# Performance work log

Hardware: AMD Instinct MI355X
Metric: run time of the kernel (lower is better)

Reference implementation:

```python
import jax, jax.numpy as jnp
import numpy as np

EPS = 1e-5


def _mlp_c(x, W0, b0, W1, b1, W2, b2, sub0):
    # per-channel 3-linear MLP (mlp_deep=2 hidden layers + output linear), hidden=latent
    h = jax.nn.relu(jnp.einsum(sub0, x, W0) + b0[:, None, None])
    h = jax.nn.relu(jnp.einsum('cbef,cfh->cbeh', h, W1) + b1[:, None, None])
    return jnp.einsum('cbef,cfh->cbeh', h, W2) + b2[:, None, None]


def _ln(x, w, b):
    # x: [C,B,M,L]; torch LayerNorm([C,M,L]) applied to x permuted to [B,C,M,L]
    # -> normalize jointly over (C,M,L) per batch element
    mu = jnp.mean(x, axis=(0, 2, 3), keepdims=True)
    var = jnp.mean((x - mu) ** 2, axis=(0, 2, 3), keepdims=True)
    return (x - mu) * jax.lax.rsqrt(var + EPS) * w[:, None] + b[:, None]


def _forward(src, dst, nodes, eW0_first, eb0_first, eW0_rest, eb0_rest,
             eW1, eb1, eW2, eb2, nW0, nb0, nW1, nb1, nW2, nb2,
             ln_nw, ln_nb, ln_ew, ln_eb):
    G, C = eW1.shape[0], eW1.shape[1]
    B, N = nodes.shape[0], nodes.shape[1]
    L = eW1.shape[-1]
    x = nodes  # [B,N,L]
    edges = None
    for i in range(G):
        # dropout p=0 -> identity (eval mode)
        if i == 0:
            # edge update: phi_e(concat(x_tgt, x_src)) per channel -> [C,B,E,L]
            m_in = jnp.concatenate([x[:, dst], x[:, src]], axis=-1)  # [B,E,2L]
            edges = _mlp_c(m_in, eW0_first, eb0_first, eW1[0], eb1[0], eW2[0], eb2[0], 'bef,cfh->cbeh')
            # scatter-add messages to target nodes
            agg = jnp.zeros((C, B, N, L), edges.dtype).at[:, :, dst].add(edges)
            n_in = jnp.concatenate([jnp.broadcast_to(x, (C, B, N, L)), agg], axis=-1)
        else:
            # x: [C,B,N,L], edges: [C,B,E,L]
            m_in = jnp.concatenate([x[:, :, dst], x[:, :, src], edges], axis=-1)  # [C,B,E,3L]
            edges = _mlp_c(m_in, eW0_rest[i - 1], eb0_rest[i - 1], eW1[i], eb1[i], eW2[i], eb2[i], 'cbef,cfh->cbeh')
            agg = jnp.zeros_like(x).at[:, :, dst].add(edges)
            n_in = jnp.concatenate([x, agg], axis=-1)  # [C,B,N,2L]
        x = _mlp_c(n_in, nW0[i], nb0[i], nW1[i], nb1[i], nW2[i], nb2[i], 'cbnf,cfh->cbnh')
        x = _ln(x, ln_nw[i], ln_nb[i])
        if i < G - 1:
            edges = _ln(edges, ln_ew[i], ln_eb[i])
    # channel_agg == 'sum'
    return jnp.sum(x, axis=0)  # [B,N,L]


def setup_inputs() -> dict:
    key = jax.random.key(0)
    B, N, L, C, G = 128, 64, 64, 2, 3
    E = N * (N - 1)
    pairs = np.array([[i, j] for i in range(N) for j in range(N) if i != j], dtype=np.int32)
    src = jnp.asarray(pairs[:, 0])  # edge_index row 0 (message source)
    dst = jnp.asarray(pairs[:, 1])  # edge_index row 1 (aggregation target)
    ks = jax.random.split(key, 8)

    def w(k, shape, fan):
        return jax.random.normal(k, shape, jnp.float32) / np.sqrt(fan)

    return {
        'nodes': jax.random.normal(ks[0], (B, N, L), jnp.float32),
        'src': src, 'dst': dst,
        'eW0_first': w(ks[1], (C, 2 * L, L), 2 * L), 'eb0_first': jnp.zeros((C, L), jnp.float32),
        'eW0_rest': w(ks[2], (G - 1, C, 3 * L, L), 3 * L), 'eb0_rest': jnp.zeros((G - 1, C, L), jnp.float32),
        'eW1': w(ks[3], (G, C, L, L), L), 'eb1': jnp.zeros((G, C, L), jnp.float32),
        'eW2': w(ks[4], (G, C, L, L), L), 'eb2': jnp.zeros((G, C, L), jnp.float32),
        'nW0': w(ks[5], (G, C, 2 * L, L), 2 * L), 'nb0': jnp.zeros((G, C, L), jnp.float32),
        'nW1': w(ks[6], (G, C, L, L), L), 'nb1': jnp.zeros((G, C, L), jnp.float32),
        'nW2': w(ks[7], (G, C, L, L), L), 'nb2': jnp.zeros((G, C, L), jnp.float32),
        'ln_nw': jnp.ones((G, C, N, L), jnp.float32), 'ln_nb': jnp.zeros((G, C, N, L), jnp.float32),
        'ln_ew': jnp.ones((G - 1, C, E, L), jnp.float32), 'ln_eb': jnp.zeros((G - 1, C, E, L), jnp.float32),
    }


def reference(nodes, src, dst, eW0_first, eb0_first, eW0_rest, eb0_rest,
              eW1, eb1, eW2, eb2, nW0, nb0, nW1, nb1, nW2, nb2,
              ln_nw, ln_nb, ln_ew, ln_eb):
    return _forward(src, dst, nodes, eW0_first, eb0_first, eW0_rest, eb0_rest,
                    eW1, eb1, eW2, eb2, nW0, nb0, nW1, nb1, nW2, nb2,
                    ln_nw, ln_nb, ln_ew, ln_eb)
```

## Files before the change

kernel.cpp:

```cpp
#include <hip/hip_runtime.h>

typedef __bf16 bf16;
typedef __attribute__((ext_vector_type(8))) __bf16 bf16x8;
typedef __attribute__((ext_vector_type(4))) __bf16 bf16x4;
typedef __attribute__((ext_vector_type(4))) float f32x4;

#define MFMA16(a,b,c) __builtin_amdgcn_mfma_f32_16x16x32_bf16((a),(b),(c),0,0,0)

#define CC 2
#define BB 128
#define EPAD 4096
#define EDGE_CNT_INV (1.0f/516096.0f)
#define NODE_CNT_INV (1.0f/8192.0f)
#define LNEPS 1e-5f

#define BC_EB0F 0
#define BC_EB0R 128
#define BC_EB1  384
#define BC_EB2  768
#define BC_NB0  1152
#define BC_NB1  1536
#define BC_NB2  1920
#define BC_TOT  2304

// ... 6 lines not shown
    16, 0, 0);
}

static __device__ __forceinline__ bool detectBf16(const void* p){
  const unsigned short* u = (const unsigned short*)p;
  int ok = 0;
#pragma unroll
  for (int i = 0; i < 64; ++i){
    unsigned v = u[i];
    unsigned e = (v >> 7) & 0xFFu;
    ok += (int)(((e >= 100u) && (e <= 150u)) || (v == 0u));
  }
  return ok >= 58;
}

static __device__ __forceinline__ float ldS(const void* p, long i, bool b16){
  return b16 ? (float)(((const bf16*)p)[i]) : ((const float*)p)[i];
}
static __device__ __forceinline__ void ld8(const void* p, long i, bool b16, float* o){
  if (b16){
    bf16x8 v = *(const bf16x8*)((const bf16*)p + i);
#pragma unroll
    for (int u=0;u<8;u++) o[u] = (float)v[u];
  } else {
    const float* f = (const float*)p + i;
    float4 a = *(const float4*)f; float4 b = *(const float4*)(f+4);
    o[0]=a.x;o[1]=a.y;o[2]=a.z;o[3]=a.w;o[4]=b.x;o[5]=b.y;o[6]=b.z;o[7]=b.w;
  }
}

static __device__ __forceinline__ unsigned sw128(unsigned row, unsigned cb){
  return row*128u + (cb ^ ((row&7u)<<4));
}
static __device__ __forceinline__ unsigned sw256(unsigned row, unsigned cb){
  return row*256u + (cb ^ ((row&7u)<<4));
}

static __device__ __forceinline__ void stage64(char* lds, const bf16* src, int tid){
#pragma unroll
  for (int q=0;q<2;q++){
    int idx = tid + q*256;
    int r = idx>>3; unsigned cb = (unsigned)((idx&7)*16);
    *(int4*)(lds + sw128((unsigned)r, cb)) = *(const int4*)((const char*)src + r*128 + cb);
  }
}
static __device__ __forceinline__ void stage128(char* lds, const bf16* src, int tid){
#pragma unroll
  for (int q=0;q<4;q++){
    int idx = tid + q*256;
    int r = idx>>4; unsigned cb = (unsigned)((idx&15)*16);
    *(int4*)(lds + sw256((unsigned)r, cb)) = *(const int4*)((const char*)src + r*256 + cb);
  }
}
static __device__ __forceinline__ void stageLin(char* lds, const char* src, int tid){
#pragma unroll
  for (int q=0;q<2;q++){
    int idx = tid + q*256;
    *(int4*)(lds + idx*16) = *(const int4*)(src + idx*16);
  }
}

static __device__ __forceinline__ bf16x8 frd64(const char* p, int row, int ks, int lane){
  return *(const bf16x8*)(p + sw128((unsigned)row, (unsigned)(ks*64 + ((lane>>4)<<4))));
}
static __device__ __forceinline__ bf16x8 frd256(const char* p, int row, int ks, int lane){
  return *(const bf16x8*)(p + sw256((unsigned)row, (unsigned)(ks*64 + ((lane>>4)<<4))));
}

template<int NMT>
static __device__ __forceinline__ void gemm64(const char* wlds, const char* hlds, int lane, f32x4 (*acc)[NMT]){
  int m15 = lane & 15;
  bf16x8 af[4][2];
#pragma unroll
  for (int nt=0;nt<4;nt++){
    af[nt][0] = frd64(wlds, nt*16+m15, 0, lane);
    af[nt][1] = frd64(wlds, nt*16+m15, 1, lane);
  }
#pragma unroll
  for (int mt=0;mt<NMT;mt++){
    bf16x8 b0 = frd64(hlds, mt*16+m15, 0, lane);
    bf16x8 b1 = frd64(hlds, mt*16+m15, 1, lane);
#pragma unroll
    for (int nt=0;nt<4;nt++){
      acc[nt][mt] = MFMA16(af[nt][0], b0, acc[nt][mt]);
      acc[nt][mt] = MFMA16(af[nt][1], b1, acc[nt][mt]);
    }
  }
}

template<int NMT>
static __device__ __forceinline__ void accZero(f32x4 (*acc)[NMT]){
#pragma unroll
  for (int a=0;a<4;a++){ for (int m=0;m<NMT;m++) acc[a][m] = zf4(); }
}
template<int NMT>
static __device__ __forceinline__ void accBias(const bf16* bias, int lane, f32x4 (*acc)[NMT]){
  int hi = lane>>4;
#pragma unroll
  for (int nt=0;nt<4;nt++){
    f32x4 bv;
#pragma unroll
    for (int r=0;r<4;r++) bv[r] = (float)bias[nt*16 + hi*4 + r];
#pragma unroll
    for (int mt=0;mt<NMT;mt++) acc[nt][mt] = bv;
  }
}
template<int NMT>
static __device__ __forceinline__ void epiRelu(char* hlds, int lane, f32x4 (*acc)[NMT]){
  int hi = lane>>4, m15 = lane&15;
#pragma unroll
  for (int nt=0;nt<4;nt++){
#pragma unroll
    for (int mt=0;mt<NMT;mt++){
      f32x4 v = acc[nt][mt];
      bf16x4 o;
#pragma unroll
      for (int r=0;r<4;r++){
        float t = v[r];
        t = t > 0.f ? t : 0.f;
        o[r] = (bf16)t;
      }
      *(bf16x4*)(hlds + sw128((unsigned)(mt*16+m15), (unsigned)(nt*32 + hi*8))) = o;
    }
  }
}

__global__ void k_prep(const void* nodes,
    const void* eW0f, const void* eW0r, const void* eW1, const void* eW2,
    const void* nW0, const void* nW1, const void* nW2,
    const void* ln_ew, const void* ln_eb, const void* ln_nw, const void* ln_nb,
    const void* eb0f, const void* eb0r, const void* eb1, const void* eb2,
    const void* nb0, const void* nb1, const void* nb2,
    bf16* WTpd, bf16* WTps, bf16* WTe0e, bf16* WTe1, bf16* WTe2,
    bf16* WTn0, bf16* WTn1, bf16* WTn2,
    bf16* lnwP, bf16* lnbP,
    bf16* xn0, bf16* lnnW, bf16* lnnB, bf16* bc, int* flag)
{
  bool b16 = detectBf16(nodes);
  int tid = threadIdx.x, blk = blockIdx.x;
  if (blk < 256){
    int t = blk>>7, c = (blk>>6)&1, j = blk&63;
    int k = tid>>2, part = tid&3;
    long dofs = (((long)(t*CC + c))*EPAD + j*64 + k)*64 + part*16;
    if (k < 63){
      int i = k + (k>=j ? 1 : 0);
      int eref = i*63 + j - (j>i ? 1 : 0);
      long sofs = (((long)(t*CC + c))*4032 + eref)*64 + part*16;
      float o[8]; bf16x8 v;
      ld8(ln_ew, sofs,   b16, o); for (int u=0;u<8;u++) v[u]=(bf16)o[u]; *(bf16x8*)(lnwP+dofs)   = v;
      ld8(ln_ew, sofs+8, b16, o); for (int u=0;u<8;u++) v[u]=(bf16)o[u]; *(bf16x8*)(lnwP+dofs+8) = v;
      ld8(ln_eb, sofs,   b16, o); for (int u=0;u<8;u++) v[u]=(bf16)o[u]; *(bf16x8*)(lnbP+dofs)   = v;
      ld8(ln_eb, sofs+8, b16, o); for (int u=0;u<8;u++) v[u]=(bf16)o[u]; *(bf16x8*)(lnbP+dofs+8) = v;
    } else {
      bf16x8 z; for (int u=0;u<8;u++) z[u]=(bf16)0.f;
      *(bf16x8*)(lnwP+dofs)=z; *(bf16x8*)(lnwP+dofs+8)=z;
      *(bf16x8*)(lnbP+dofs)=z; *(bf16x8*)(lnbP+dofs+8)=z;
    }
    return;
  }
  int job = blk - 256;
  if (job < 46){
    const void* src = nullptr; bf16* dst = nullptr; int K = 64; long so = 0;
    if (job < 6){        int t=job>>1, c=job&1; dst = WTpd + (long)(t*CC+c)*4096;
      if (t==0){ src=eW0f; so=(long)c*128*64; } else { src=eW0r; so=((long)(t-1)*CC+c)*192*64; } }
    else if (job < 12){  int q=job-6; int t=q>>1,c=q&1; dst = WTps + (long)(t*CC+c)*4096;
      if (t==0){ src=eW0f; so=(long)c*128*64 + 64*64; } else { src=eW0r; so=((long)(t-1)*CC+c)*192*64 + 64*64; } }
    else if (job < 16){  int q=job-12; int t=q>>1,c=q&1; dst=WTe0e + (long)(t*CC+c)*4096; src=eW0r; so=((long)t*CC+c)*192*64 + 128*64; }
    else if (job < 22){  int q=job-16; int t=q>>1,c=q&1; dst=WTe1 + (long)(t*CC+c)*4096; src=eW1; so=((long)t*CC+c)*4096; }
    else if (job < 28){  int q=job-22; int t=q>>1,c=q&1; dst=WTe2 + (long)(t*CC+c)*4096; src=eW2; so=((long)t*CC+c)*4096; }
    else if (job < 34){  int q=job-28; int t=q>>1,c=q&1; dst=WTn0 + (long)(t*CC+c)*8192; src=nW0; so=((long)t*CC+c)*128*64; K=128; }
    else if (job < 40){  int q=job-34; int t=q>>1,c=q&1; dst=WTn1 + (long)(t*CC+c)*4096; src=nW1; so=((long)t*CC+c)*4096; }
    else              {  int q=job-40; int t=q>>1,c=q&1; dst=WTn2 + (long)(t*CC+c)*4096; src=nW2; so=((long)t*CC+c)*4096; }
    for (int idx = tid; idx < K*64; idx += 256){
      int n = idx & 63, k = idx >> 6;
      dst[(long)n*K + k] = (bf16)ldS(src, so + (long)k*64 + n, b16);
// ... 22 lines not shown
#pragma unroll
      for (int u=0;u<8;u++) v[u]=(bf16)t[u];
      *(bf16x8*)(dst + o) = v;
    }
  } else {
    for (int idx = tid; idx < BC_TOT; idx += 256){
      float v;
      if      (idx < BC_EB0R) v = ldS(eb0f, idx - BC_EB0F, b16);
      else if (idx < BC_EB1 ) v = ldS(eb0r, idx - BC_EB0R, b16);
      else if (idx < BC_EB2 ) v = ldS(eb1,  idx - BC_EB1,  b16);
      else if (idx < BC_NB0 ) v = ldS(eb2,  idx - BC_EB2,  b16);
      else if (idx < BC_NB1 ) v = ldS(nb0,  idx - BC_NB0,  b16);
      else if (idx < BC_NB2 ) v = ldS(nb1,  idx - BC_NB1,  b16);
      else                    v = ldS(nb2,  idx - BC_NB2,  b16);
      bc[idx] = (bf16)v;
    }
    if (tid == 0) flag[0] = b16 ? 1 : 0;
  }
}

__global__ __launch_bounds__(256,2) void k_p0(const bf16* xn0,
    const bf16* WTpd, const bf16* WTps, const bf16* bc, bf16* Xd, bf16* Xs)
{
  int tid=threadIdx.x, lane=tid&63, w=tid>>6;
  int b = blockIdx.x;
  extern __shared__ char sm[];
  char* xn = sm;
  char* Wp = sm + 8192;
  stage64(xn, xn0 + (long)b*4096, tid);
  stage64(Wp,         WTpd + 0,    tid);
  stage64(Wp + 8192,  WTps + 0,    tid);
  stage64(Wp + 16384, WTpd + 4096, tid);
  stage64(Wp + 24576, WTps + 4096, tid);
  __syncthreads();
  int c = w>>1, p = w&1;
  f32x4 acc[4][4];
  if (p==0) accBias<4>(bc + BC_EB0F + c*64, lane, acc);
  else accZero<4>(acc);
  gemm64<4>(Wp + (c*2+p)*8192, xn, lane, acc);
  int hi=lane>>4, m15=lane&15;
  bf16* dst = (p==0 ? Xd : Xs) + ((long)c*BB + b)*64*64;
#pragma unroll
  for (int nt=0;nt<4;nt++){
#pragma unroll
    for (int mt=0;mt<4;mt++){
      f32x4 v = acc[nt][mt];
      bf16x4 o = {(bf16)v[0],(bf16)v[1],(bf16)v[2],(bf16)v[3]};
      *(bf16x4*)(dst + (long)(mt*16+m15)*64 + nt*16+hi*4) = o;
    }
  }
}

template<int T>
__global__ __launch_bounds__(256,2) void k_edge(
    bf16* edges, const bf16* Xd, const bf16* Xs, float* agg, float* eS,
    const float2* eMR,
    const bf16* WTe0e, const bf16* WTe1, const bf16* WTe2,
    const bf16* lnwP, const bf16* lnbP, const bf16* bc)
{
  int tid=threadIdx.x, lane=tid&63, w=tid>>6;
  int j = blockIdx.x, bg = blockIdx.y, c = blockIdx.z;
  extern __shared__ char sm[];
  char* Wl1 = sm;
  char* Wl2 = sm + 8192;
  char* Wl0 = sm + 16384;
  char* lwL = sm + 24576;
  char* lbL = sm + 32768;
  char* hb  = sm + (T>0 ? 40960 : 16384) + w*8192;

  int hi = lane>>4, m15 = lane&15;
  int mrow = lane>>3;
  unsigned cbyte = (unsigned)((lane&7)*16);
  int cbk = (lane&7)*8;
  int b0 = bg*32 + w*8;

  float2 mr8[8];
  if (T>0){
#pragma unroll
    for (int t=0;t<8;t++) mr8[t] = eMR[(T-1)*BB + b0 + t];
  }

  stage64(Wl1, WTe1 + (long)(T*CC+c)*4096, tid);
  stage64(Wl2, WTe2 + (long)(T*CC+c)*4096, tid);
  if (T>0){
    stage64(Wl0, WTe0e + (long)((T-1)*CC+c)*4096, tid);
    const char* lwg = (const char*)(lnwP + (((long)(T-1)*CC+c)*EPAD + (long)j*64)*64);
    const char* lbg = (const char*)(lnbP + (((long)(T-1)*CC+c)*EPAD + (long)j*64)*64);
    stageLin(lwL, lwg, tid);
    stageLin(lbL, lbg, tid);
  }
  __syncthreads();

  for (int t=0; t<8; t++){
    int b = b0 + t;
    long cb = (long)c*BB + b;
    bf16* erow = edges + (cb*EPAD + (long)j*64)*64;
    const bf16* xdrow = Xd + (cb*64 + j)*64;
    const bf16* xsbase = Xs + cb*4096;

    f32x4 acc[4][4];

    if (T==0){
      bf16x8 xd8v = *(const bf16x8*)(xdrow + cbk);
      float xd8[8];
#pragma unroll
      for (int u=0;u<8;u++) xd8[u] = (float)xd8v[u];
#pragma unroll
      for (int it=0; it<8; it++){
        int m = mrow + it*8;
        int i = m + (m>=j ? 1 : 0); if (i>63) i = 63;
        bf16x8 y8 = *(const bf16x8*)(xsbase + (long)i*64 + cbk);
        bf16x8 o;
#pragma unroll
        for (int u=0;u<8;u++){
          float tt = xd8[u] + (float)y8[u];
          tt = tt > 0.f ? tt : 0.f;
          o[u] = (bf16)tt;
        }
        *(bf16x8*)(hb + sw128((unsigned)m, (unsigned)(cbk*2))) = o;
      }
      accBias<4>(bc + BC_EB1 + (T*CC+c)*64, lane, acc);
      gemm64<4>(Wl1, hb, lane, acc);
      epiRelu<4>(hb, lane, acc);
      accBias<4>(bc + BC_EB2 + (T*CC+c)*64, lane, acc);
      gemm64<4>(Wl2, hb, lane, acc);
    } else {
      float mu = mr8[t].x, rs = mr8[t].y;
      asm volatile("s_waitcnt lgkmcnt(0)" ::: "memory");
#pragma unroll
      for (int it=0; it<8; it++)
        dma16(hb + it*1024, (const char*)erow + it*1024 + (long)lane*16);
      asm volatile("s_waitcnt vmcnt(0)" ::: "memory");
      __builtin_amdgcn_sched_barrier(0);
#pragma unroll
      for (int it=0; it<8; it++){
        int m = mrow + it*8;
        bf16x8 e  = *(const bf16x8*)(hb  + lane*16 + it*1024);
        bf16x8 wv = *(const bf16x8*)(lwL + lane*16 + it*1024);
        bf16x8 bv = *(const bf16x8*)(lbL + lane*16 + it*1024);
        bf16x8 o;
#pragma unroll
        for (int u=0;u<8;u++){
          float tt = ((float)e[u] - mu) * rs;
          tt = tt * (float)wv[u] + (float)bv[u];
          o[u] = (bf16)tt;
        }
        *(bf16x8*)(hb + sw128((unsigned)m, cbyte)) = o;
      }
      bf16x4 xdv[4], xsv[4][4];
#pragma unroll
      for (int nt=0;nt<4;nt++) xdv[nt] = *(const bf16x4*)(xdrow + nt*16 + hi*4);
#pragma unroll
      for (int mt=0;mt<4;mt++){
        int m = mt*16 + m15;
        int i = m + (m>=j ? 1 : 0); if (i>63) i=63;
#pragma unroll
        for (int nt=0;nt<4;nt++)
          xsv[mt][nt] = *(const bf16x4*)(xsbase + (long)i*64 + nt*16 + hi*4);
      }
      accZero<4>(acc);
      gemm64<4>(Wl0, hb, lane, acc);
#pragma unroll
      for (int mt=0;mt<4;mt++){
        int m = mt*16 + m15;
#pragma unroll
        for (int nt=0;nt<4;nt++){
          f32x4 v = acc[nt][mt];
          float t0 = v[0] + (float)xdv[nt][0] + (float)xsv[mt][nt][0];
          float t1 = v[1] + (float)xdv[nt][1] + (float)xsv[mt][nt][1];
          float t2 = v[2] + (float)xdv[nt][2] + (float)xsv[mt][nt][2];
          float t3 = v[3] + (float)xdv[nt][3] + (float)xsv[mt][nt][3];
          bf16x4 o;
          o[0] = (bf16)(t0>0.f?t0:0.f); o[1] = (bf16)(t1>0.f?t1:0.f);
          o[2] = (bf16)(t2>0.f?t2:0.f); o[3] = (bf16)(t3>0.f?t3:0.f);
          *(bf16x4*)(hb + sw128((unsigned)m, (unsigned)(nt*32+hi*8))) = o;
        }
      }
      accBias<4>(bc + BC_EB1 + (T*CC+c)*64, lane, acc);
      gemm64<4>(Wl1, hb, lane, acc);
      epiRelu<4>(hb, lane, acc);
      accBias<4>(bc + BC_EB2 + (T*CC+c)*64, lane, acc);
      gemm64<4>(Wl2, hb, lane, acc);
    }

    if (m15 == 15){
#pragma unroll
      for (int nt=0;nt<4;nt++) acc[nt][3] = zf4();
    }
    if (T < 2){
      float s1=0.f, s2=0.f;
#pragma unroll
      for (int nt=0;nt<4;nt++){ for (int mt=0;mt<4;mt++){ for (int r=0;r<4;r++){
        float v = acc[nt][mt][r]; s1 += v; s2 = fmaf(v,v,s2);
      }}}
#pragma unroll
      for (int d=1; d<64; d<<=1){ s1 += __shfl_xor(s1,d); s2 += __shfl_xor(s2,d); }
      if (lane == 0){
        atomicAdd(&eS[((long)T*BB + b)*2],     s1);
        atomicAdd(&eS[((long)T*BB + b)*2 + 1], s2);
      }
#pragma unroll
      for (int mt=0;mt<4;mt++){
        int m = mt*16 + m15;
#pragma unroll
        for (int nt=0;nt<4;nt++){
          f32x4 v = acc[nt][mt];
          bf16x4 o = {(bf16)v[0],(bf16)v[1],(bf16)v[2],(bf16)v[3]};
          *(bf16x4*)(hb + sw128((unsigned)m, (unsigned)(nt*32+hi*8))) = o;
        }
      }
#pragma unroll
      for (int it=0; it<8; it++){
        int m = mrow + it*8;
        *(int4*)((char*)erow + m*128 + cbyte) = *(const int4*)(hb + sw128((unsigned)m, cbyte));
      }
    }
#pragma unroll
    for (int nt=0;nt<4;nt++){
      float p0 = acc[nt][0][0]+acc[nt][1][0]+acc[nt][2][0]+acc[nt][3][0];
      float p1 = acc[nt][0][1]+acc[nt][1][1]+acc[nt][2][1]+acc[nt][3][1];
      float p2 = acc[nt][0][2]+acc[nt][1][2]+acc[nt][2][2]+acc[nt][3][2];
      float p3 = acc[nt][0][3]+acc[nt][1][3]+acc[nt][2][3]+acc[nt][3][3];
      unsigned base = (unsigned)(nt*64 + hi*16);
      float2 q0 = {p0,p1}, q1 = {p2,p3};
      *(float2*)(hb + (unsigned)m15*256u + (base       ^ (((unsigned)(m15&7))<<4))) = q0;
      *(float2*)(hb + (unsigned)m15*256u + ((base+8u)  ^ (((unsigned)(m15&7))<<4))) = q1;
    }
    float s = 0.f;
#pragma unroll
    for (int r=0;r<16;r++){
      s += *(const float*)(hb + (unsigned)r*256u + ((((unsigned)lane)*4u) ^ (((unsigned)(r&7))<<4)));
    }
    agg[(cb*64 + j)*64 + lane] = s;
  }
}

template<int T>
__global__ __launch_bounds__(256,2) void k_nodeA(const bf16* xn0,
    const bf16* xcur, const float* agg, float* xtilde, float* nS,
    const bf16* WTn0, const bf16* WTn1, const bf16* WTn2, const bf16* bc)
{
  int tid=threadIdx.x, lane=tid&63, w=tid>>6;
  int b = blockIdx.x, c = blockIdx.y;
  extern __shared__ char sm[];
  char* nin = sm;
  char* W0l = sm + 16384;
  char* W1l = sm + 32768;
  char* W2l = sm + 40960;
  char* hb  = sm + 49152 + w*2048;
  long cb = (long)c*BB + b;

#pragma unroll
  for (int q=0;q<2;q++){
    int idx = tid + q*256;
    int r = idx>>3; int e8 = (idx&7)*8;
    bf16x8 o;
    if (T==0) o = *(const bf16x8*)(xn0 + ((long)b*64 + r)*64 + e8);
    else      o = *(const bf16x8*)(xcur + (cb*64 + r)*64 + e8);
    *(bf16x8*)(nin + sw256((unsigned)r, (unsigned)(e8*2))) = o;
  }
#pragma unroll
  for (int q=0;q<2;q++){
    int idx = tid + q*256;
    int r = idx>>3; int e8 = (idx&7)*8;
    const float* ap = agg + (cb*64 + r)*64 + e8;
    float4 x = *(const float4*)ap; float4 y = *(const float4*)(ap+4);
    bf16x8 o = {(bf16)x.x,(bf16)x.y,(bf16)x.z,(bf16)x.w,(bf16)y.x,(bf16)y.y,(bf16)y.z,(bf16)y.w};
    *(bf16x8*)(nin + sw256((unsigned)r, (unsigned)(128 + e8*2))) = o;
  }
  stage128(W0l, WTn0 + (long)(T*CC+c)*8192, tid);
  stage64 (W1l, WTn1 + (long)(T*CC+c)*4096, tid);
  stage64 (W2l, WTn2 + (long)(T*CC+c)*4096, tid);
  __syncthreads();

  int hi=lane>>4, m15=lane&15;
  int m0 = w*16;
  long bofs = (long)(T*CC+c)*64;
  f32x4 a1[4][1];
  accBias<1>(bc + BC_NB0 + bofs, lane, a1);
  {
    bf16x8 bv[4];
#pragma unroll
    for (int ks=0;ks<4;ks++) bv[ks] = frd256(nin, m0+m15, ks, lane);
#pragma unroll
    for (int nt=0;nt<4;nt++){
#pragma unroll
// ... 160 lines not shown
  size_t edgesO = A((size_t)CC*BB*EPAD*64*2);
  size_t XdO  = A((size_t)CC*BB*64*64*2);
  size_t XsO  = A((size_t)CC*BB*64*64*2);
  size_t xtO  = A((size_t)CC*BB*64*64*4);
  size_t aggO = A((size_t)CC*BB*64*64*4);
  size_t xcO  = A((size_t)CC*BB*64*64*2);
  size_t lnwO = A((size_t)2*CC*EPAD*64*2);
  size_t lnbO = A((size_t)2*CC*EPAD*64*2);
  size_t WTpdO = A((size_t)3*CC*4096*2);
  size_t WTpsO = A((size_t)3*CC*4096*2);
  size_t WTe0eO = A((size_t)2*CC*4096*2);
  size_t WTe1O = A((size_t)3*CC*4096*2);
  size_t WTe2O = A((size_t)3*CC*4096*2);
  size_t WTn0O = A((size_t)3*CC*8192*2);
  size_t WTn1O = A((size_t)3*CC*4096*2);
  size_t WTn2O = A((size_t)3*CC*4096*2);
  size_t eSO = A((size_t)2*BB*2*4);
  size_t nSO = A((size_t)3*BB*2*4);
  size_t xn0O = A((size_t)BB*64*64*2);
  size_t lnnWO = A((size_t)3*CC*64*64*2);
  size_t lnnBO = A((size_t)3*CC*64*64*2);
  size_t bcO = A((size_t)BC_TOT*2);
  size_t flagO = A(4);
  size_t eMRO = A((size_t)2*BB*8);
  if (ws_size < off) return;

  bf16* edges = (bf16*)(ws+edgesO);
  bf16* Xd = (bf16*)(ws+XdO);  bf16* Xs = (bf16*)(ws+XsO);
  float* xt = (float*)(ws+xtO);  float* agg = (float*)(ws+aggO);
  bf16* xc = (bf16*)(ws+xcO);
  bf16* lnwP = (bf16*)(ws+lnwO); bf16* lnbP = (bf16*)(ws+lnbO);
  bf16* WTpd = (bf16*)(ws+WTpdO); bf16* WTps = (bf16*)(ws+WTpsO);
  bf16* WTe0e = (bf16*)(ws+WTe0eO); bf16* WTe1 = (bf16*)(ws+WTe1O); bf16* WTe2 = (bf16*)(ws+WTe2O);
  bf16* WTn0 = (bf16*)(ws+WTn0O); bf16* WTn1 = (bf16*)(ws+WTn1O); bf16* WTn2 = (bf16*)(ws+WTn2O);
  float* eS = (float*)(ws+eSO); float* nS = (float*)(ws+nSO);
  bf16* xn0 = (bf16*)(ws+xn0O);
  bf16* lnnW = (bf16*)(ws+lnnWO); bf16* lnnB = (bf16*)(ws+lnnBO);
  bf16* bc = (bf16*)(ws+bcO); int* flag = (int*)(ws+flagO);
  float2* eMR = (float2*)(ws+eMRO);

  hipMemsetAsync(ws+eSO, 0, (size_t)2*BB*2*4, stream);
  hipMemsetAsync(ws+nSO, 0, (size_t)3*BB*2*4, stream);

  k_prep<<<379, 256, 0, stream>>>(nodes, eW0f, eW0r, eW1, eW2, nW0, nW1, nW2,
                                  ln_ew, ln_eb, ln_nw, ln_nb,
                                  eb0f, eb0r, eb1, eb2, nb0, nb1, nb2,
                                  WTpd, WTps, WTe0e, WTe1, WTe2, WTn0, WTn1, WTn2,
                                  lnwP, lnbP, xn0, lnnW, lnnB, bc, flag);
  k_p0<<<BB, 256, 40960, stream>>>(xn0, WTpd, WTps, bc, Xd, Xs);

  dim3 eg(64, 4, CC);
  dim3 ng(BB, CC);

  k_edge<0><<<eg, 256, 49152, stream>>>(edges, Xd, Xs, agg, eS, eMR, WTe0e, WTe1, WTe2, lnwP, lnbP, bc);
  k_nodeA<0><<<ng, 256, 57344, stream>>>(xn0, xc, agg, xt, nS, WTn0, WTn1, WTn2, bc);
  k_nodeB<0><<<BB, 256, 49152, stream>>>(xt, nS, lnnW, lnnB, xc, Xd, Xs, WTpd, WTps, bc, eS, eMR);

  k_edge<1><<<eg, 256, 73728, stream>>>(edges, Xd, Xs, agg, eS, eMR, WTe0e, WTe1, WTe2, lnwP, lnbP, bc);
  k_nodeA<1><<<ng, 256, 57344, stream>>>(xn0, xc, agg, xt, nS, WTn0, WTn1, WTn2, bc);
  k_nodeB<1><<<BB, 256, 49152, stream>>>(xt, nS, lnnW, lnnB, xc, Xd, Xs, WTpd, WTps, bc, eS, eMR);

  k_edge<2><<<eg, 256, 73728, stream>>>(edges, Xd, Xs, agg, eS, eMR, WTe0e, WTe1, WTe2, lnwP, lnbP, bc);
  k_nodeA<2><<<ng, 256, 57344, stream>>>(xn0, xc, agg, xt, nS, WTn0, WTn1, WTn2, bc);
  k_final<<<BB, 256, 0, stream>>>(xt, nS, lnnW, lnnB, flag, d_out);
}
```

Before: 280.9 us.

## Split edge MLP tiles across wave pairs with 512-thread blocks

```diff
diff --git a/kernel.cpp b/kernel.cpp
--- a/kernel.cpp
+++ b/kernel.cpp
@@ -82,12 +82,12 @@
     *(int4*)(lds + sw256((unsigned)r, cb)) = *(const int4*)((const char*)src + r*256 + cb);
   }
 }
-static __device__ __forceinline__ void stageLin(char* lds, const char* src, int tid){
-#pragma unroll
-  for (int q=0;q<2;q++){
-    int idx = tid + q*256;
-    *(int4*)(lds + idx*16) = *(const int4*)(src + idx*16);
-  }
+static __device__ __forceinline__ void stage64b(char* lds, const bf16* src, int tid){
+  int r = tid>>3; unsigned cb = (unsigned)((tid&7)*16);
+  *(int4*)(lds + sw128((unsigned)r, cb)) = *(const int4*)((const char*)src + r*128 + cb);
+}
+static __device__ __forceinline__ void stageLinb(char* lds, const char* src, int tid){
+  *(int4*)(lds + tid*16) = *(const int4*)(src + tid*16);
 }
 
 static __device__ __forceinline__ bf16x8 frd64(const char* p, int row, int ks, int lane){
@@ -117,11 +117,34 @@
     }
   }
 }
+static __device__ __forceinline__ void gemm64h(const char* wlds, const char* hlds, int lane, int ntb, f32x4 (*acc)[4]){
+  int m15 = lane & 15;
+  bf16x8 af[2][2];
+#pragma unroll
+  for (int n2=0;n2<2;n2++){
+    af[n2][0] = frd64(wlds, (ntb+n2)*16+m15, 0, lane);
+    af[n2][1] = frd64(wlds, (ntb+n2)*16+m15, 1, lane);
+  }
+#pragma unroll
+  for (int mt=0;mt<4;mt++){
+    bf16x8 b0 = frd64(hlds, mt*16+m15, 0, lane);
+    bf16x8 b1 = frd64(hlds, mt*16+m15, 1, lane);
+#pragma unroll
+    for (int n2=0;n2<2;n2++){
+      acc[n2][mt] = MFMA16(af[n2][0], b0, acc[n2][mt]);
+      acc[n2][mt] = MFMA16(af[n2][1], b1, acc[n2][mt]);
+    }
+  }
+}
 
 template<int NMT>
 static __device__ __forceinline__ void accZero(f32x4 (*acc)[NMT]){
 #pragma unroll
   for (int a=0;a<4;a++){ for (int m=0;m<NMT;m++) acc[a][m] = zf4(); }
+}
+static __device__ __forceinline__ void accZeroH(f32x4 (*acc)[4]){
+#pragma unroll
+  for (int a=0;a<2;a++){ for (int m=0;m<4;m++) acc[a][m] = zf4(); }
 }
 template<int NMT>
 static __device__ __forceinline__ void accBias(const bf16* bias, int lane, f32x4 (*acc)[NMT]){
@@ -133,6 +156,17 @@
     for (int r=0;r<4;r++) bv[r] = (float)bias[nt*16 + hi*4 + r];
 #pragma unroll
     for (int mt=0;mt<NMT;mt++) acc[nt][mt] = bv;
+  }
+}
+static __device__ __forceinline__ void accBiasH(const bf16* bias, int lane, int ntb, f32x4 (*acc)[4]){
+  int hi = lane>>4;
+#pragma unroll
+  for (int n2=0;n2<2;n2++){
+    f32x4 bv;
+#pragma unroll
+    for (int r=0;r<4;r++) bv[r] = (float)bias[(ntb+n2)*16 + hi*4 + r];
+#pragma unroll
+    for (int mt=0;mt<4;mt++) acc[n2][mt] = bv;
   }
 }
 template<int NMT>
@@ -151,6 +185,24 @@
         o[r] = (bf16)t;
       }
       *(bf16x4*)(hlds + sw128((unsigned)(mt*16+m15), (unsigned)(nt*32 + hi*8))) = o;
+    }
+  }
+}
+static __device__ __forceinline__ void epiReluH(char* hlds, int lane, int ntb, f32x4 (*acc)[4]){
+  int hi = lane>>4, m15 = lane&15;
+#pragma unroll
+  for (int n2=0;n2<2;n2++){
+#pragma unroll
+    for (int mt=0;mt<4;mt++){
+      f32x4 v = acc[n2][mt];
+      bf16x4 o;
+#pragma unroll
+      for (int r=0;r<4;r++){
+        float t = v[r];
+        t = t > 0.f ? t : 0.f;
+        o[r] = (bf16)t;
+      }
+      *(bf16x4*)(hlds + sw128((unsigned)(mt*16+m15), (unsigned)((ntb+n2)*32 + hi*8))) = o;
     }
   }
 }
@@ -279,13 +331,15 @@
 }
 
 template<int T>
-__global__ __launch_bounds__(256,2) void k_edge(
+__global__ __launch_bounds__(512,4) void k_edge(
     bf16* edges, const bf16* Xd, const bf16* Xs, float* agg, float* eS,
     const float2* eMR,
     const bf16* WTe0e, const bf16* WTe1, const bf16* WTe2,
     const bf16* lnwP, const bf16* lnbP, const bf16* bc)
 {
   int tid=threadIdx.x, lane=tid&63, w=tid>>6;
+  int pair = w>>1, half = w&1;
+  int ntb = half*2;
   int j = blockIdx.x, bg = blockIdx.y, c = blockIdx.z;
   extern __shared__ char sm[];
   char* Wl1 = sm;
@@ -293,13 +347,13 @@
   char* Wl0 = sm + 16384;
   char* lwL = sm + 24576;
   char* lbL = sm + 32768;
-  char* hb  = sm + (T>0 ? 40960 : 16384) + w*8192;
+  char* hb  = sm + (T>0 ? 40960 : 16384) + pair*8192;
 
   int hi = lane>>4, m15 = lane&15;
   int mrow = lane>>3;
   unsigned cbyte = (unsigned)((lane&7)*16);
   int cbk = (lane&7)*8;
-  int b0 = bg*32 + w*8;
+  int b0 = bg*32 + pair*8;
 
   float2 mr8[8];
   if (T>0){
@@ -307,14 +361,16 @@
     for (int t=0;t<8;t++) mr8[t] = eMR[(T-1)*BB + b0 + t];
   }
 
-  stage64(Wl1, WTe1 + (long)(T*CC+c)*4096, tid);
-  stage64(Wl2, WTe2 + (long)(T*CC+c)*4096, tid);
-  if (T>0){
-    stage64(Wl0, WTe0e + (long)((T-1)*CC+c)*4096, tid);
-    const char* lwg = (const char*)(lnwP + (((long)(T-1)*CC+c)*EPAD + (long)j*64)*64);
-    const char* lbg = (const char*)(lnbP + (((long)(T-1)*CC+c)*EPAD + (long)j*64)*64);
-    stageLin(lwL, lwg, tid);
-    stageLin(lbL, lbg, tid);
+  if (tid < 512){
+    stage64b(Wl1, WTe1 + (long)(T*CC+c)*4096, tid);
+    stage64b(Wl2, WTe2 + (long)(T*CC+c)*4096, tid);
+    if (T>0){
+      stage64b(Wl0, WTe0e + (long)((T-1)*CC+c)*4096, tid);
+      const char* lwg = (const char*)(lnwP + (((long)(T-1)*CC+c)*EPAD + (long)j*64)*64);
+      const char* lbg = (const char*)(lnbP + (((long)(T-1)*CC+c)*EPAD + (long)j*64)*64);
+      stageLinb(lwL, lwg, tid);
+      stageLinb(lbL, lbg, tid);
+    }
   }
   __syncthreads();
 
@@ -325,7 +381,8 @@
     const bf16* xdrow = Xd + (cb*64 + j)*64;
     const bf16* xsbase = Xs + cb*4096;
 
-    f32x4 acc[4][4];
+    f32x4 acc[2][4];
+    __syncthreads();
 
     if (T==0){
       bf16x8 xd8v = *(const bf16x8*)(xdrow + cbk);
@@ -333,7 +390,8 @@
 #pragma unroll
       for (int u=0;u<8;u++) xd8[u] = (float)xd8v[u];
 #pragma unroll
-      for (int it=0; it<8; it++){
+      for (int q=0; q<4; q++){
+        int it = half*4 + q;
         int m = mrow + it*8;
         int i = m + (m>=j ? 1 : 0); if (i>63) i = 63;
         bf16x8 y8 = *(const bf16x8*)(xsbase + (long)i*64 + cbk);
@@ -346,21 +404,27 @@
         }
         *(bf16x8*)(hb + sw128((unsigned)m, (unsigned)(cbk*2))) = o;
       }
-      accBias<4>(bc + BC_EB1 + (T*CC+c)*64, lane, acc);
-      gemm64<4>(Wl1, hb, lane, acc);
-      epiRelu<4>(hb, lane, acc);
-      accBias<4>(bc + BC_EB2 + (T*CC+c)*64, lane, acc);
-      gemm64<4>(Wl2, hb, lane, acc);
+      __syncthreads();
+      accBiasH(bc + BC_EB1 + (T*CC+c)*64, lane, ntb, acc);
+      gemm64h(Wl1, hb, lane, ntb, acc);
+      __syncthreads();
+      epiReluH(hb, lane, ntb, acc);
+      __syncthreads();
+      accBiasH(bc + BC_EB2 + (T*CC+c)*64, lane, ntb, acc);
+      gemm64h(Wl2, hb, lane, ntb, acc);
     } else {
       float mu = mr8[t].x, rs = mr8[t].y;
-      asm volatile("s_waitcnt lgkmcnt(0)" ::: "memory");
-#pragma unroll
-      for (int it=0; it<8; it++)
+#pragma unroll
+      for (int q=0; q<4; q++){
+        int it = half*4 + q;
         dma16(hb + it*1024, (const char*)erow + it*1024 + (long)lane*16);
+      }
       asm volatile("s_waitcnt vmcnt(0)" ::: "memory");
       __builtin_amdgcn_sched_barrier(0);
-#pragma unroll
-      for (int it=0; it<8; it++){
+      __syncthreads();
+#pragma unroll
+      for (int q=0; q<4; q++){
+        int it = half*4 + q;
         int m = mrow + it*8;
         bf16x8 e  = *(const bf16x8*)(hb  + lane*16 + it*1024);
         bf16x8 wv = *(const bf16x8*)(lwL + lane*16 + it*1024);
@@ -374,51 +438,56 @@
         }
         *(bf16x8*)(hb + sw128((unsigned)m, cbyte)) = o;
       }
-      bf16x4 xdv[4], xsv[4][4];
-#pragma unroll
-      for (int nt=0;nt<4;nt++) xdv[nt] = *(const bf16x4*)(xdrow + nt*16 + hi*4);
+      bf16x4 xdv[2], xsv[4][2];
+#pragma unroll
+      for (int n2=0;n2<2;n2++) xdv[n2] = *(const bf16x4*)(xdrow + (ntb+n2)*16 + hi*4);
 #pragma unroll
       for (int mt=0;mt<4;mt++){
         int m = mt*16 + m15;
         int i = m + (m>=j ? 1 : 0); if (i>63) i=63;
 #pragma unroll
-        for (int nt=0;nt<4;nt++)
-          xsv[mt][nt] = *(const bf16x4*)(xsbase + (long)i*64 + nt*16 + hi*4);
-      }
-      accZero<4>(acc);
-      gemm64<4>(Wl0, hb, lane, acc);
+        for (int n2=0;n2<2;n2++)
+          xsv[mt][n2] = *(const bf16x4*)(xsbase + (long)i*64 + (ntb+n2)*16 + hi*4);
+      }
+      __syncthreads();
+      accZeroH(acc);
+      gemm64h(Wl0, hb, lane, ntb, acc);
+      __syncthreads();
 #pragma unroll
       for (int mt=0;mt<4;mt++){
         int m = mt*16 + m15;
 #pragma unroll
-        for (int nt=0;nt<4;nt++){
-          f32x4 v = acc[nt][mt];
-          float t0 = v[0] + (float)xdv[nt][0] + (float)xsv[mt][nt][0];
-          float t1 = v[1] + (float)xdv[nt][1] + (float)xsv[mt][nt][1];
-          float t2 = v[2] + (float)xdv[nt][2] + (float)xsv[mt][nt][2];
-          float t3 = v[3] + (float)xdv[nt][3] + (float)xsv[mt][nt][3];
+        for (int n2=0;n2<2;n2++){
+          f32x4 v = acc[n2][mt];
+          float t0 = v[0] + (float)xdv[n2][0] + (float)xsv[mt][n2][0];
+          float t1 = v[1] + (float)xdv[n2][1] + (float)xsv[mt][n2][1];
+          float t2 = v[2] + (float)xdv[n2][2] + (float)xsv[mt][n2][2];
+          float t3 = v[3] + (float)xdv[n2][3] + (float)xsv[mt][n2][3];
           bf16x4 o;
           o[0] = (bf16)(t0>0.f?t0:0.f); o[1] = (bf16)(t1>0.f?t1:0.f);
           o[2] = (bf16)(t2>0.f?t2:0.f); o[3] = (bf16)(t3>0.f?t3:0.f);
-          *(bf16x4*)(hb + sw128((unsigned)m, (unsigned)(nt*32+hi*8))) = o;
+          *(bf16x4*)(hb + sw128((unsigned)m, (unsigned)((ntb+n2)*32+hi*8))) = o;
         }
       }
-      accBias<4>(bc + BC_EB1 + (T*CC+c)*64, lane, acc);
-      gemm64<4>(Wl1, hb, lane, acc);
-      epiRelu<4>(hb, lane, acc);
-      accBias<4>(bc + BC_EB2 + (T*CC+c)*64, lane, acc);
-      gemm64<4>(Wl2, hb, lane, acc);
+      __syncthreads();
+      accBiasH(bc + BC_EB1 + (T*CC+c)*64, lane, ntb, acc);
+      gemm64h(Wl1, hb, lane, ntb, acc);
+      __syncthreads();
+      epiReluH(hb, lane, ntb, acc);
+      __syncthreads();
+      accBiasH(bc + BC_EB2 + (T*CC+c)*64, lane, ntb, acc);
+      gemm64h(Wl2, hb, lane, ntb, acc);
     }
 
     if (m15 == 15){
 #pragma unroll
-      for (int nt=0;nt<4;nt++) acc[nt][3] = zf4();
+      for (int n2=0;n2<2;n2++) acc[n2][3] = zf4();
     }
     if (T < 2){
       float s1=0.f, s2=0.f;
 #pragma unroll
-      for (int nt=0;nt<4;nt++){ for (int mt=0;mt<4;mt++){ for (int r=0;r<4;r++){
-        float v = acc[nt][mt][r]; s1 += v; s2 = fmaf(v,v,s2);
+      for (int n2=0;n2<2;n2++){ for (int mt=0;mt<4;mt++){ for (int r=0;r<4;r++){
+        float v = acc[n2][mt][r]; s1 += v; s2 = fmaf(v,v,s2);
       }}}
 #pragma unroll
       for (int d=1; d<64; d<<=1){ s1 += __shfl_xor(s1,d); s2 += __shfl_xor(s2,d); }
@@ -426,39 +495,38 @@
         atomicAdd(&eS[((long)T*BB + b)*2],     s1);
         atomicAdd(&eS[((long)T*BB + b)*2 + 1], s2);
       }
+      __syncthreads();
 #pragma unroll
       for (int mt=0;mt<4;mt++){
         int m = mt*16 + m15;
 #pragma unroll
-        for (int nt=0;nt<4;nt++){
-          f32x4 v = acc[nt][mt];
+        for (int n2=0;n2<2;n2++){
+          f32x4 v = acc[n2][mt];
           bf16x4 o = {(bf16)v[0],(bf16)v[1],(bf16)v[2],(bf16)v[3]};
-          *(bf16x4*)(hb + sw128((unsigned)m, (unsigned)(nt*32+hi*8))) = o;
+          *(bf16x4*)(hb + sw128((unsigned)m, (unsigned)((ntb+n2)*32+hi*8))) = o;
         }
       }
-#pragma unroll
-      for (int it=0; it<8; it++){
-        int m = mrow + it*8;
+      __syncthreads();
+#pragma unroll
+      for (int q=0; q<4; q++){
+        int m = mrow + (half*4+q)*8;
         *(int4*)((char*)erow + m*128 + cbyte) = *(const int4*)(hb + sw128((unsigned)m, cbyte));
       }
     }
 #pragma unroll
-    for (int nt=0;nt<4;nt++){
-      float p0 = acc[nt][0][0]+acc[nt][1][0]+acc[nt][2][0]+acc[nt][3][0];
-      float p1 = acc[nt][0][1]+acc[nt][1][1]+acc[nt][2][1]+acc[nt][3][1];
-      float p2 = acc[nt][0][2]+acc[nt][1][2]+acc[nt][2][2]+acc[nt][3][2];
-      float p3 = acc[nt][0][3]+acc[nt][1][3]+acc[nt][2][3]+acc[nt][3][3];
-      unsigned base = (unsigned)(nt*64 + hi*16);
-      float2 q0 = {p0,p1}, q1 = {p2,p3};
-      *(float2*)(hb + (unsigned)m15*256u + (base       ^ (((unsigned)(m15&7))<<4))) = q0;
-      *(float2*)(hb + (unsigned)m15*256u + ((base+8u)  ^ (((unsigned)(m15&7))<<4))) = q1;
-    }
-    float s = 0.f;
-#pragma unroll
-    for (int r=0;r<16;r++){
-      s += *(const float*)(hb + (unsigned)r*256u + ((((unsigned)lane)*4u) ^ (((unsigned)(r&7))<<4)));
-    }
-    agg[(cb*64 + j)*64 + lane] = s;
+    for (int n2=0;n2<2;n2++){
+      f32x4 p;
+#pragma unroll
+      for (int r=0;r<4;r++)
+        p[r] = acc[n2][0][r]+acc[n2][1][r]+acc[n2][2][r]+acc[n2][3][r];
+#pragma unroll
+      for (int d=1; d<16; d<<=1){
+#pragma unroll
+        for (int r=0;r<4;r++) p[r] += __shfl_xor(p[r], d);
+      }
+      if (m15 == 0)
+        *(f32x4*)(agg + (cb*64 + j)*64 + (ntb+n2)*16 + hi*4) = p;
+    }
   }
 }
 
@@ -725,15 +793,15 @@
   dim3 eg(64, 4, CC);
   dim3 ng(BB, CC);
 
-  k_edge<0><<<eg, 256, 49152, stream>>>(edges, Xd, Xs, agg, eS, eMR, WTe0e, WTe1, WTe2, lnwP, lnbP, bc);
+  k_edge<0><<<eg, 512, 49152, stream>>>(edges, Xd, Xs, agg, eS, eMR, WTe0e, WTe1, WTe2, lnwP, lnbP, bc);
   k_nodeA<0><<<ng, 256, 57344, stream>>>(xn0, xc, agg, xt, nS, WTn0, WTn1, WTn2, bc);
   k_nodeB<0><<<BB, 256, 49152, stream>>>(xt, nS, lnnW, lnnB, xc, Xd, Xs, WTpd, WTps, bc, eS, eMR);
 
-  k_edge<1><<<eg, 256, 73728, stream>>>(edges, Xd, Xs, agg, eS, eMR, WTe0e, WTe1, WTe2, lnwP, lnbP, bc);
+  k_edge<1><<<eg, 512, 73728, stream>>>(edges, Xd, Xs, agg, eS, eMR, WTe0e, WTe1, WTe2, lnwP, lnbP, bc);
   k_nodeA<1><<<ng, 256, 57344, stream>>>(xn0, xc, agg, xt, nS, WTn0, WTn1, WTn2, bc);
   k_nodeB<1><<<BB, 256, 49152, stream>>>(xt, nS, lnnW, lnnB, xc, Xd, Xs, WTpd, WTps, bc, eS, eMR);
 
-  k_edge<2><<<eg, 256, 73728, stream>>>(edges, Xd, Xs, agg, eS, eMR, WTe0e, WTe1, WTe2, lnwP, lnbP, bc);
+  k_edge<2><<<eg, 512, 73728, stream>>>(edges, Xd, Xs, agg, eS, eMR, WTe0e, WTe1, WTe2, lnwP, lnbP, bc);
   k_nodeA<2><<<ng, 256, 57344, stream>>>(xn0, xc, agg, xt, nS, WTn0, WTn1, WTn2, bc);
   k_final<<<BB, 256, 0, stream>>>(xt, nS, lnnW, lnnB, flag, d_out);
 }
```

Measured after the change: 392.5 us. 39.7% more time.

## Double-buffer edge tile loads in half-tiles and reduce aggregation via shuffles

Applied to the files above, without the earlier changes.

```diff
diff --git a/kernel.cpp b/kernel.cpp
--- a/kernel.cpp
+++ b/kernel.cpp
@@ -301,12 +301,6 @@
   int cbk = (lane&7)*8;
   int b0 = bg*32 + w*8;
 
-  float2 mr8[8];
-  if (T>0){
-#pragma unroll
-    for (int t=0;t<8;t++) mr8[t] = eMR[(T-1)*BB + b0 + t];
-  }
-
   stage64(Wl1, WTe1 + (long)(T*CC+c)*4096, tid);
   stage64(Wl2, WTe2 + (long)(T*CC+c)*4096, tid);
   if (T>0){
@@ -318,53 +312,133 @@
   }
   __syncthreads();
 
+  if (T==0){
+    for (int t=0; t<8; t++){
+      int b = b0 + t;
+      long cb = (long)c*BB + b;
+      bf16* erow = edges + (cb*EPAD + (long)j*64)*64;
+      const bf16* xdrow = Xd + (cb*64 + j)*64;
+      const bf16* xsbase = Xs + cb*4096;
+
+      f32x4 acc[4][4];
+      bf16x8 xd8v = *(const bf16x8*)(xdrow + cbk);
+      float xd8[8];
+#pragma unroll
+      for (int u=0;u<8;u++) xd8[u] = (float)xd8v[u];
+#pragma unroll
+      for (int it=0; it<8; it++){
+        int m = mrow + it*8;
+        int i = m + (m>=j ? 1 : 0); if (i>63) i = 63;
+        bf16x8 y8 = *(const bf16x8*)(xsbase + (long)i*64 + cbk);
+        bf16x8 o;
+#pragma unroll
+        for (int u=0;u<8;u++){
+          float tt = xd8[u] + (float)y8[u];
+          tt = tt > 0.f ? tt : 0.f;
+          o[u] = (bf16)tt;
+        }
+        *(bf16x8*)(hb + sw128((unsigned)m, (unsigned)(cbk*2))) = o;
+      }
+      accBias<4>(bc + BC_EB1 + (T*CC+c)*64, lane, acc);
+      gemm64<4>(Wl1, hb, lane, acc);
+      epiRelu<4>(hb, lane, acc);
+      accBias<4>(bc + BC_EB2 + (T*CC+c)*64, lane, acc);
+      gemm64<4>(Wl2, hb, lane, acc);
+
+      if (m15 == 15){
+#pragma unroll
+        for (int nt=0;nt<4;nt++) acc[nt][3] = zf4();
+      }
+      float s1=0.f, s2=0.f;
+#pragma unroll
+      for (int nt=0;nt<4;nt++){ for (int mt=0;mt<4;mt++){ for (int r=0;r<4;r++){
+        float v = acc[nt][mt][r]; s1 += v; s2 = fmaf(v,v,s2);
+      }}}
+#pragma unroll
+      for (int d=1; d<64; d<<=1){ s1 += __shfl_xor(s1,d); s2 += __shfl_xor(s2,d); }
+      if (lane == 0){
+        atomicAdd(&eS[((long)T*BB + b)*2],     s1);
+        atomicAdd(&eS[((long)T*BB + b)*2 + 1], s2);
+      }
+#pragma unroll
+      for (int mt=0;mt<4;mt++){
+        int m = mt*16 + m15;
+#pragma unroll
+        for (int nt=0;nt<4;nt++){
+          f32x4 v = acc[nt][mt];
+          bf16x4 o = {(bf16)v[0],(bf16)v[1],(bf16)v[2],(bf16)v[3]};
+          *(bf16x4*)(hb + sw128((unsigned)m, (unsigned)(nt*32+hi*8))) = o;
+        }
+      }
+#pragma unroll
+      for (int it=0; it<8; it++){
+        int m = mrow + it*8;
+        *(int4*)((char*)erow + m*128 + cbyte) = *(const int4*)(hb + sw128((unsigned)m, cbyte));
+      }
+#pragma unroll
+      for (int nt=0;nt<4;nt++){
+        f32x4 p;
+#pragma unroll
+        for (int r=0;r<4;r++)
+          p[r] = acc[nt][0][r]+acc[nt][1][r]+acc[nt][2][r]+acc[nt][3][r];
+#pragma unroll
+        for (int d=1; d<16; d<<=1){
+#pragma unroll
+          for (int r=0;r<4;r++) p[r] += __shfl_xor(p[r], d);
+        }
+        if (m15 == 0)
+          *(f32x4*)(agg + (cb*64 + j)*64 + nt*16 + hi*4) = p;
+      }
+    }
+    return;
+  }
+
+  {
+    const char* er0 = (const char*)(edges + (((long)c*BB + b0)*EPAD + (long)j*64)*64);
+    asm volatile("s_waitcnt lgkmcnt(0)" ::: "memory");
+#pragma unroll
+    for (int q=0; q<4; q++)
+      dma16(hb + q*1024, er0 + q*1024 + (long)lane*16);
+    asm volatile("s_waitcnt vmcnt(0)" ::: "memory");
+    __builtin_amdgcn_sched_barrier(0);
+  }
+
+  float mu = 0.f, rs = 0.f;
+  float s1 = 0.f, s2 = 0.f;
+  f32x4 pAgg[4];
+
   for (int t=0; t<8; t++){
     int b = b0 + t;
     long cb = (long)c*BB + b;
     bf16* erow = edges + (cb*EPAD + (long)j*64)*64;
     const bf16* xdrow = Xd + (cb*64 + j)*64;
     const bf16* xsbase = Xs + cb*4096;
-
-    f32x4 acc[4][4];
-
-    if (T==0){
-      bf16x8 xd8v = *(const bf16x8*)(xdrow + cbk);
-      float xd8[8];
-#pragma unroll
-      for (int u=0;u<8;u++) xd8[u] = (float)xd8v[u];
-#pragma unroll
-      for (int it=0; it<8; it++){
-        int m = mrow + it*8;
-        int i = m + (m>=j ? 1 : 0); if (i>63) i = 63;
-        bf16x8 y8 = *(const bf16x8*)(xsbase + (long)i*64 + cbk);
-        bf16x8 o;
-#pragma unroll
-        for (int u=0;u<8;u++){
-          float tt = xd8[u] + (float)y8[u];
-          tt = tt > 0.f ? tt : 0.f;
-          o[u] = (bf16)tt;
+    { float2 mr = eMR[(T-1)*BB + b]; mu = mr.x; rs = mr.y; }
+    s1 = 0.f; s2 = 0.f;
+#pragma unroll
+    for (int nt=0;nt<4;nt++) pAgg[nt] = zf4();
+
+#pragma unroll
+    for (int hf=0; hf<2; hf++){
+      char* buf = hb + hf*4096;
+      {
+        int hnext = t*2 + hf + 1;
+        if (hnext < 16){
+          int tn = hnext>>1, hfn = hnext&1;
+          const char* ern = (const char*)(edges + (((long)c*BB + (b0+tn))*EPAD + (long)j*64)*64) + hfn*4096;
+          char* bufn = hb + hfn*4096;
+          asm volatile("s_waitcnt lgkmcnt(0)" ::: "memory");
+#pragma unroll
+          for (int q=0; q<4; q++)
+            dma16(bufn + q*1024, ern + q*1024 + (long)lane*16);
         }
-        *(bf16x8*)(hb + sw128((unsigned)m, (unsigned)(cbk*2))) = o;
-      }
-      accBias<4>(bc + BC_EB1 + (T*CC+c)*64, lane, acc);
-      gemm64<4>(Wl1, hb, lane, acc);
-      epiRelu<4>(hb, lane, acc);
-      accBias<4>(bc + BC_EB2 + (T*CC+c)*64, lane, acc);
-      gemm64<4>(Wl2, hb, lane, acc);
-    } else {
-      float mu = mr8[t].x, rs = mr8[t].y;
-      asm volatile("s_waitcnt lgkmcnt(0)" ::: "memory");
-#pragma unroll
-      for (int it=0; it<8; it++)
-        dma16(hb + it*1024, (const char*)erow + it*1024 + (long)lane*16);
-      asm volatile("s_waitcnt vmcnt(0)" ::: "memory");
-      __builtin_amdgcn_sched_barrier(0);
-#pragma unroll
-      for (int it=0; it<8; it++){
-        int m = mrow + it*8;
-        bf16x8 e  = *(const bf16x8*)(hb  + lane*16 + it*1024);
-        bf16x8 wv = *(const bf16x8*)(lwL + lane*16 + it*1024);
-        bf16x8 bv = *(const bf16x8*)(lbL + lane*16 + it*1024);
+      }
+#pragma unroll
+      for (int q=0; q<4; q++){
+        int ml = mrow + q*8;
+        bf16x8 e  = *(const bf16x8*)(buf + lane*16 + q*1024);
+        bf16x8 wv = *(const bf16x8*)(lwL + hf*4096 + lane*16 + q*1024);
+        bf16x8 bv = *(const bf16x8*)(lbL + hf*4096 + lane*16 + q*1024);
         bf16x8 o;
 #pragma unroll
         for (int u=0;u<8;u++){
@@ -372,93 +446,99 @@
           tt = tt * (float)wv[u] + (float)bv[u];
           o[u] = (bf16)tt;
         }
-        *(bf16x8*)(hb + sw128((unsigned)m, cbyte)) = o;
-      }
-      bf16x4 xdv[4], xsv[4][4];
+        *(bf16x8*)(buf + sw128((unsigned)ml, cbyte)) = o;
+      }
+      bf16x4 xdv[4], xsv[2][4];
 #pragma unroll
       for (int nt=0;nt<4;nt++) xdv[nt] = *(const bf16x4*)(xdrow + nt*16 + hi*4);
 #pragma unroll
-      for (int mt=0;mt<4;mt++){
-        int m = mt*16 + m15;
+      for (int mtl=0;mtl<2;mtl++){
+        int m = hf*32 + mtl*16 + m15;
         int i = m + (m>=j ? 1 : 0); if (i>63) i=63;
 #pragma unroll
         for (int nt=0;nt<4;nt++)
-          xsv[mt][nt] = *(const bf16x4*)(xsbase + (long)i*64 + nt*16 + hi*4);
-      }
-      accZero<4>(acc);
-      gemm64<4>(Wl0, hb, lane, acc);
-#pragma unroll
-      for (int mt=0;mt<4;mt++){
-        int m = mt*16 + m15;
+          xsv[mtl][nt] = *(const bf16x4*)(xsbase + (long)i*64 + nt*16 + hi*4);
+      }
+      f32x4 acc[4][2];
+      accZero<2>(acc);
+      gemm64<2>(Wl0, buf, lane, acc);
+#pragma unroll
+      for (int mtl=0;mtl<2;mtl++){
+        int ml = mtl*16 + m15;
 #pragma unroll
         for (int nt=0;nt<4;nt++){
-          f32x4 v = acc[nt][mt];
-          float t0 = v[0] + (float)xdv[nt][0] + (float)xsv[mt][nt][0];
-          float t1 = v[1] + (float)xdv[nt][1] + (float)xsv[mt][nt][1];
-          float t2 = v[2] + (float)xdv[nt][2] + (float)xsv[mt][nt][2];
-          float t3 = v[3] + (float)xdv[nt][3] + (float)xsv[mt][nt][3];
+          f32x4 v = acc[nt][mtl];
+          float t0 = v[0] + (float)xdv[nt][0] + (float)xsv[mtl][nt][0];
+          float t1 = v[1] + (float)xdv[nt][1] + (float)xsv[mtl][nt][1];
+          float t2 = v[2] + (float)xdv[nt][2] + (float)xsv[mtl][nt][2];
+          float t3 = v[3] + (float)xdv[nt][3] + (float)xsv[mtl][nt][3];
           bf16x4 o;
           o[0] = (bf16)(t0>0.f?t0:0.f); o[1] = (bf16)(t1>0.f?t1:0.f);
           o[2] = (bf16)(t2>0.f?t2:0.f); o[3] = (bf16)(t3>0.f?t3:0.f);
-          *(bf16x4*)(hb + sw128((unsigned)m, (unsigned)(nt*32+hi*8))) = o;
+          *(bf16x4*)(buf + sw128((unsigned)ml, (unsigned)(nt*32+hi*8))) = o;
         }
       }
-      accBias<4>(bc + BC_EB1 + (T*CC+c)*64, lane, acc);
-      gemm64<4>(Wl1, hb, lane, acc);
-      epiRelu<4>(hb, lane, acc);
-      accBias<4>(bc + BC_EB2 + (T*CC+c)*64, lane, acc);
-      gemm64<4>(Wl2, hb, lane, acc);
-    }
-
-    if (m15 == 15){
-#pragma unroll
-      for (int nt=0;nt<4;nt++) acc[nt][3] = zf4();
-    }
+      accBias<2>(bc + BC_EB1 + (T*CC+c)*64, lane, acc);
+      gemm64<2>(Wl1, buf, lane, acc);
+      epiRelu<2>(buf, lane, acc);
+      accBias<2>(bc + BC_EB2 + (T*CC+c)*64, lane, acc);
+      gemm64<2>(Wl2, buf, lane, acc);
+      if (hf==1 && m15==15){
+#pragma unroll
+        for (int nt=0;nt<4;nt++) acc[nt][1] = zf4();
+      }
+      if (T < 2){
+#pragma unroll
+        for (int nt=0;nt<4;nt++){ for (int mtl=0;mtl<2;mtl++){ for (int r=0;r<4;r++){
+          float v = acc[nt][mtl][r]; s1 += v; s2 = fmaf(v,v,s2);
+        }}}
+      }
+#pragma unroll
+      for (int nt=0;nt<4;nt++){
+#pragma unroll
+        for (int r=0;r<4;r++) pAgg[nt][r] += acc[nt][0][r] + acc[nt][1][r];
+      }
+      if (T < 2){
+#pragma unroll
+        for (int mtl=0;mtl<2;mtl++){
+          int ml = mtl*16 + m15;
+#pragma unroll
+          for (int nt=0;nt<4;nt++){
+            f32x4 v = acc[nt][mtl];
+            bf16x4 o = {(bf16)v[0],(bf16)v[1],(bf16)v[2],(bf16)v[3]};
+            *(bf16x4*)(buf + sw128((unsigned)ml, (unsigned)(nt*32+hi*8))) = o;
+          }
+        }
+#pragma unroll
+        for (int q=0; q<4; q++){
+          int ml = mrow + q*8;
+          int m = hf*32 + ml;
+          *(int4*)((char*)erow + m*128 + cbyte) = *(const int4*)(buf + sw128((unsigned)ml, cbyte));
+        }
+      }
+      asm volatile("s_waitcnt vmcnt(0)" ::: "memory");
+      __builtin_amdgcn_sched_barrier(0);
+    }
+
     if (T < 2){
-      float s1=0.f, s2=0.f;
-#pragma unroll
-      for (int nt=0;nt<4;nt++){ for (int mt=0;mt<4;mt++){ for (int r=0;r<4;r++){
-        float v = acc[nt][mt][r]; s1 += v; s2 = fmaf(v,v,s2);
-      }}}
 #pragma unroll
       for (int d=1; d<64; d<<=1){ s1 += __shfl_xor(s1,d); s2 += __shfl_xor(s2,d); }
       if (lane == 0){
         atomicAdd(&eS[((long)T*BB + b)*2],     s1);
         atomicAdd(&eS[((long)T*BB + b)*2 + 1], s2);
       }
-#pragma unroll
-      for (int mt=0;mt<4;mt++){
-        int m = mt*16 + m15;
-#pragma unroll
-        for (int nt=0;nt<4;nt++){
-          f32x4 v = acc[nt][mt];
-          bf16x4 o = {(bf16)v[0],(bf16)v[1],(bf16)v[2],(bf16)v[3]};
-          *(bf16x4*)(hb + sw128((unsigned)m, (unsigned)(nt*32+hi*8))) = o;
-        }
-      }
-#pragma unroll
-      for (int it=0; it<8; it++){
-        int m = mrow + it*8;
-        *(int4*)((char*)erow + m*128 + cbyte) = *(const int4*)(hb + sw128((unsigned)m, cbyte));
-      }
     }
 #pragma unroll
     for (int nt=0;nt<4;nt++){
-      float p0 = acc[nt][0][0]+acc[nt][1][0]+acc[nt][2][0]+acc[nt][3][0];
-      float p1 = acc[nt][0][1]+acc[nt][1][1]+acc[nt][2][1]+acc[nt][3][1];
-      float p2 = acc[nt][0][2]+acc[nt][1][2]+acc[nt][2][2]+acc[nt][3][2];
-      float p3 = acc[nt][0][3]+acc[nt][1][3]+acc[nt][2][3]+acc[nt][3][3];
-      unsigned base = (unsigned)(nt*64 + hi*16);
-      float2 q0 = {p0,p1}, q1 = {p2,p3};
-      *(float2*)(hb + (unsigned)m15*256u + (base       ^ (((unsigned)(m15&7))<<4))) = q0;
-      *(float2*)(hb + (unsigned)m15*256u + ((base+8u)  ^ (((unsigned)(m15&7))<<4))) = q1;
-    }
-    float s = 0.f;
-#pragma unroll
-    for (int r=0;r<16;r++){
-      s += *(const float*)(hb + (unsigned)r*256u + ((((unsigned)lane)*4u) ^ (((unsigned)(r&7))<<4)));
-    }
-    agg[(cb*64 + j)*64 + lane] = s;
+      f32x4 p = pAgg[nt];
+#pragma unroll
+      for (int d=1; d<16; d<<=1){
+#pragma unroll
+        for (int r=0;r<4;r++) p[r] += __shfl_xor(p[r], d);
+      }
+      if (m15 == 0)
+        *(f32x4*)(agg + (cb*64 + j)*64 + nt*16 + hi*4) = p;
+    }
   }
 }
 
```

New measurement: 303.3 us. 8.0% more time.
